# Kernel tuning notes

Hardware: AMD Instinct MI355X
Metric: run time of the kernel (lower is better)

Reference implementation:

```python
import jax, jax.numpy as jnp
import numpy as np

B, G, A = 8, 32768, 64          # molecules, grid points/molecule, atomic orbitals/molecule
N_ORB, DIM, L_FUNC, N_OUT = 400, 128, 3, 1
EPS = 1e-12


def setup_inputs() -> dict:
    key = jax.random.key(0)
    ks = jax.random.split(key, 12)
    # interatomic/grid distances in Bohr-ish range (strictly positive)
    distance_matrices = jax.random.uniform(ks[0], (B, G, A), jnp.float32) * 10.0 + 0.05
    quantum_numbers = jax.random.randint(ks[1], (B, A), 0, 3, jnp.int32)   # q-1 in {0,1,2}
    atomic_orbitals = jax.random.randint(ks[2], (B, A), 0, N_ORB, jnp.int32)
    N_electrons = jax.random.uniform(ks[3], (B,), jnp.float32) * 50.0 + 10.0
    coef_table = jax.random.normal(ks[4], (N_ORB, DIM), jnp.float32) * 0.1
    zeta_table = jnp.ones((N_ORB, 1), jnp.float32)   # nn.init.ones_
    W_pre_w = jax.random.normal(ks[5], (DIM, 1), jnp.float32) * 0.1
    W_pre_b = jax.random.normal(ks[6], (DIM,), jnp.float32) * 0.01
    W_func_w = jax.random.normal(ks[7], (L_FUNC, DIM, DIM), jnp.float32) * (1.0 / np.sqrt(DIM))
    W_func_b = jax.random.normal(ks[8], (L_FUNC, DIM), jnp.float32) * 0.01
    W_prop_w = jax.random.normal(ks[9], (N_OUT, DIM), jnp.float32) * (1.0 / np.sqrt(DIM))
    W_prop_b = jax.random.normal(ks[10], (N_OUT,), jnp.float32) * 0.01
    return dict(distance_matrices=distance_matrices, quantum_numbers=quantum_numbers,
                atomic_orbitals=atomic_orbitals, N_electrons=N_electrons,
                coef_table=coef_table, zeta_table=zeta_table,
                W_pre_w=W_pre_w, W_pre_b=W_pre_b,
                W_func_w=W_func_w, W_func_b=W_func_b,
                W_prop_w=W_prop_w, W_prop_b=W_prop_b)


def reference(distance_matrices, quantum_numbers, atomic_orbitals, N_electrons,
              coef_table, zeta_table, W_pre_w, W_pre_b, W_func_w, W_func_b,
              W_prop_w, W_prop_b):
    d = distance_matrices                                   # [B,G,A]
    q = quantum_numbers.astype(jnp.float32) + 1.0           # principal quantum number {1,2,3}
    z = zeta_table[atomic_orbitals][..., 0]                 # [B,A] orbital exponents
    # GTO basis: d^(q-1) * exp(-(z*d)^2); block-diagonal padding (d=1e6 -> 0) is
    # equivalent to this batched per-molecule form.
    gto = d ** (q[:, None, :] - 1.0) * jnp.exp(-(z[:, None, :] * d) ** 2)
    gto = gto / jnp.maximum(jnp.sqrt(jnp.sum(gto * gto, 1, keepdims=True)), EPS)
    # per-molecule L2-normalized LCAO coefficients (F.normalize over AO axis)
    c = coef_table[atomic_orbitals]                         # [B,A,D]
    c = c / jnp.maximum(jnp.sqrt(jnp.sum(c * c, 1, keepdims=True)), EPS)
    # LCAO: molecular orbitals, then per-molecule normalization over grid points
    mo = jnp.einsum('bga,bad->bgd', gto, c)                 # [B,G,D]
    mo = mo / jnp.maximum(jnp.sqrt(jnp.sum(mo * mo, 1, keepdims=True)), EPS)
    mo = jnp.sqrt(N_electrons / DIM)[:, None, None] * mo
    densities = jnp.sum(mo * mo, -1, keepdims=True)         # [B,G,1]
    # DNN-based energy functional
    v = densities * W_pre_w[:, 0] + W_pre_b                 # [B,G,D]  (Linear(1,dim))
    for l in range(L_FUNC):
        v = jax.nn.relu(jnp.einsum('bgd,ed->bge', v, W_func_w[l]) + W_func_b[l])
    final = jnp.sum(v, 1)                                   # operation == 'sum' over grid
    E_xcH = final @ W_prop_w.T + W_prop_b                   # [B,N_OUT]
    return E_xcH
```

## Files before the change

### kernel.cpp

```cpp
#include <hip/hip_runtime.h>
#include <stdint.h>


#define BB 8
#define GG 32768
#define AA 64
#define DD 128
#define EPSF 1e-12f

#define WS_M    0u
#define WS_ZQ   131072u
#define WS_CN   135168u
#define WS_UW   397312u
#define WS_CCT  398336u
#define WS_W2   529408u
#define WS_W3   562176u
#define WS_DENS 594944u
#define WS_M8   1643520u
#define WS_GTO  2692096u
#define WS_END  36246528u

typedef __attribute__((ext_vector_type(8))) short bf16x8;
typedef __attribute__((ext_vector_type(4))) float f32x4;

__device__ __forceinline__ unsigned short f2bf(float f) {
    union { float f; unsigned int u; } x; x.f = f;
    unsigned int u = x.u + 0x7FFFu + ((x.u >> 16) & 1u);
    return (unsigned short)(u >> 16);
}
__device__ __forceinline__ float bfround(float f) {
    union { float f; unsigned int u; } x; x.f = f;
    unsigned int u = x.u + 0x7FFFu + ((x.u >> 16) & 1u);
    x.u = u & 0xFFFF0000u;
    return x.f;
}
__device__ __forceinline__ float gto_eval(float dv, float zz, float qm) {
    float ttv = zz * dv;
    float ex = __expf(-ttv * ttv);
    float pw = (qm < 0.5f) ? 1.f : ((qm < 1.5f) ? dv : dv * dv);
    return pw * ex;
}

__global__ __launch_bounds__(256)
void k_prep(const int* __restrict__ q, const int* __restrict__ ao,
            const float* __restrict__ coef, const float* __restrict__ zeta,
            const float* __restrict__ wfunc_w, const float* __restrict__ wprop_b,
            float* __restrict__ out, char* __restrict__ ws)
{
    int tid = blockIdx.x * 256 + threadIdx.x;
    if (tid < 32768) {
        int lsel = tid >> 14;
        int idx = tid & 16383;
        unsigned short* dst = (unsigned short*)(ws + (lsel == 0 ? WS_W2 : WS_W3));
        dst[idx] = f2bf(wfunc_w[(lsel + 1) * 16384 + idx]);
    } else if (tid < 33792) {
        int i = tid - 32768;
        int b = i >> 7, dd = i & 127;
        float s = 0.f;
        for (int a = 0; a < AA; ++a) {
            float v = coef[ao[b * AA + a] * DD + dd];
            s += v * v;
        }
        float inv = 1.f / fmaxf(sqrtf(s), EPSF);
        float* cn = (float*)(ws + WS_CN);
        for (int a = 0; a < AA; ++a)
            cn[((size_t)b * AA + a) * DD + dd] = coef[ao[b * AA + a] * DD + dd] * inv;
    } else if (tid < 34304) {
        int i = tid - 33792;
        int b = i >> 6, a = i & 63;
        float* zq = (float*)(ws + WS_ZQ);
        zq[b * 128 + a]      = zeta[ao[b * AA + a]];
        zq[b * 128 + 64 + a] = (float)q[b * AA + a];
    } else if (tid < 34312) {
        out[tid - 34304] = wprop_b[0];
    } else if (tid < 67080) {
        ((float*)(ws + WS_M))[tid - 34312] = 0.f;
    }
}

__global__ __launch_bounds__(1024)
void k_corr2(const float* __restrict__ wpre_w, const float* __restrict__ wpre_b,
             const float* __restrict__ wfunc_w, const float* __restrict__ wfunc_b,
             const float* __restrict__ wprop_w, float* __restrict__ out,
             char* __restrict__ ws)
{
    __shared__ float v1e[128], v1b[128], v2e[128], v2b[128];
    __shared__ float red;
    const int t = threadIdx.x, e = t >> 3, s = t & 7;
    if (t == 0) red = 0.f;
    float* uw = (float*)(ws + WS_UW);

    float su = 0.f, sw = 0.f;
    {
        const float* W1r = wfunc_w + e * 128 + s * 16;
        const float* pw  = wpre_w + s * 16;
        const float* pb  = wpre_b + s * 16;
        #pragma unroll
        for (int k = 0; k < 4; ++k) {
            float4 wv = *(const float4*)(W1r + k * 4);
            float4 a  = *(const float4*)(pw + k * 4);
            float4 bq = *(const float4*)(pb + k * 4);
            su += wv.x * a.x + wv.y * a.y + wv.z * a.z + wv.w * a.w;
            sw += wv.x * bq.x + wv.y * bq.y + wv.z * bq.z + wv.w * bq.w;
        }
    }
    #pragma unroll
    for (int m = 1; m < 8; m <<= 1) { su += __shfl_xor(su, m); sw += __shfl_xor(sw, m); }
    if (s == 0) {
        float w0 = sw + wfunc_b[e];
        uw[e] = su; uw[128 + e] = w0;
        float r = fmaxf(w0, 0.f);
        v1e[e] = r; v1b[e] = bfround(r);
    }
    __syncthreads();

    float ze = 0.f, zb = 0.f;
    {
        const float* W2r = wfunc_w + 16384 + e * 128 + s * 16;
        #pragma unroll
        for (int k = 0; k < 16; ++k) {
            float wv = W2r[k];
            ze += wv * v1e[s * 16 + k];
            zb += bfround(wv) * v1b[s * 16 + k];
        }
    }
    #pragma unroll
    for (int m = 1; m < 8; m <<= 1) { ze += __shfl_xor(ze, m); zb += __shfl_xor(zb, m); }
    if (s == 0) {
        float bias = wfunc_b[128 + e];
        v2e[e] = fmaxf(ze + bias, 0.f);
        v2b[e] = bfround(fmaxf(zb + bias, 0.f));
    }
    __syncthreads();

    float ye = 0.f, yb = 0.f;
    {
        const float* W3r = wfunc_w + 32768 + e * 128 + s * 16;
        #pragma unroll
        for (int k = 0; k < 16; ++k) {
            float wv = W3r[k];
            ye += wv * v2e[s * 16 + k];
            yb += bfround(wv) * v2b[s * 16 + k];
        }
    }
    #pragma unroll
    for (int m = 1; m < 8; m <<= 1) { ye += __shfl_xor(ye, m); yb += __shfl_xor(yb, m); }
    if (s == 0) {
        float bias = wfunc_b[256 + e];
        float diff = (fmaxf(ye + bias, 0.f) - fmaxf(yb + bias, 0.f)) * wprop_w[e];
        atomicAdd(&red, diff);
    }
    __syncthreads();
    if (t == 0) {
        float corr = red * (float)GG;
        #pragma unroll
        for (int b = 0; b < BB; ++b) atomicAdd(&out[b], corr);
    }
}

template<int NREP, bool STORE>
__global__ __launch_bounds__(256, 4)
void k_gto(const float* __restrict__ dmat, char* __restrict__ ws)
{
    __shared__ unsigned short gs[2][8192];
    const int b = blockIdx.y;
    const int chunk = blockIdx.x;
    const int t = threadIdx.x;
    const int g4 = t & 31, a8 = t >> 5;
    const int wv = t >> 6, l = t & 63;
    const int lrow = l & 15, lk = l >> 4;

    const float* zzp = (const float*)(ws + WS_ZQ) + b * 128;
    float4 za = *(const float4*)(zzp + a8 * 8);
    float4 zbv = *(const float4*)(zzp + a8 * 8 + 4);
    float4 qa = *(const float4*)(zzp + 64 + a8 * 8);
    float4 qb = *(const float4*)(zzp + 64 + a8 * 8 + 4);
    float zz8[8] = {za.x, za.y, za.z, za.w, zbv.x, zbv.y, zbv.z, zbv.w};
    float qm8[8] = {qa.x, qa.y, qa.z, qa.w, qb.x, qb.y, qb.z, qb.w};

    const float* dbase = dmat + ((size_t)b * GG + (size_t)chunk * 256) * AA;
    unsigned short* gto = (unsigned short*)(ws + WS_GTO);

    #pragma unroll
    for (int tt = 0; tt < 2; ++tt) {
        float gv[4][8];
        #pragma unroll
        for (int gg = 0; gg < 4; ++gg) {
            const float* rp = dbase + (size_t)(tt * 128 + g4 * 4 + gg) * AA + a8 * 8;
            float4 x0 = *(const float4*)rp;
            float4 x1 = *(const float4*)(rp + 4);
            float dv8[8] = {x0.x, x0.y, x0.z, x0.w, x1.x, x1.y, x1.z, x1.w};
            #pragma unroll
            for (int j = 0; j < 8; ++j) gv[gg][j] = gto_eval(dv8[j], zz8[j], qm8[j]);
        }
        #pragma unroll
        for (int j = 0; j < 8; ++j) {
            int a = a8 * 8 + j;
            unsigned int lo = (unsigned int)f2bf(gv[0][j]) | ((unsigned int)f2bf(gv[1][j]) << 16);
            unsigned int hi = (unsigned int)f2bf(gv[2][j]) | ((unsigned int)f2bf(gv[3][j]) << 16);
            *(uint2*)((char*)gs[tt] + a * 256 + ((g4 * 8) ^ ((a & 15) << 4))) = make_uint2(lo, hi);
        }
        if (STORE) {
            #pragma unroll
            for (int gg = 0; gg < 4; ++gg) {
                unsigned int w0 = (unsigned int)f2bf(gv[gg][0]) | ((unsigned int)f2bf(gv[gg][1]) << 16);
                unsigned int w1 = (unsigned int)f2bf(gv[gg][2]) | ((unsigned int)f2bf(gv[gg][3]) << 16);
                unsigned int w2 = (unsigned int)f2bf(gv[gg][4]) | ((unsigned int)f2bf(gv[gg][5]) << 16);
                unsigned int w3 = (unsigned int)f2bf(gv[gg][6]) | ((unsigned int)f2bf(gv[gg][7]) << 16);
                size_t go = ((size_t)b * GG + (size_t)chunk * 256 + tt * 128 + g4 * 4 + gg) * AA + a8 * 8;
                *(uint4*)(gto + go) = make_uint4(w0, w1, w2, w3);
            }
        }
    }
    __syncthreads();

    f32x4 acc[4];
    #pragma unroll
    for (int rb = 0; rb < 4; ++rb) acc[rb] = (f32x4){0.f, 0.f, 0.f, 0.f};
    #pragma unroll
    for (int tt = 0; tt < 2; ++tt)
        #pragma unroll
        for (int kt = 0; kt < 4; ++kt) {
            int colB = kt * 64 + lk * 16;
            int ra = wv * 16 + lrow;
            bf16x8 af = *(const bf16x8*)((const char*)gs[tt] + ra * 256 + (colB ^ ((ra & 15) << 4)));
            #pragma unroll
            for (int rb = 0; rb < 4; ++rb) {
                int rr = rb * 16 + lrow;
                bf16x8 bv = *(const bf16x8*)((const char*)gs[tt] + rr * 256 + (colB ^ ((rr & 15) << 4)));
                acc[rb] = __builtin_amdgcn_mfma_f32_16x16x32_bf16(af, bv, acc[rb], 0, 0, 0);
            }
        }

    float* Mg = (float*)(ws + (NREP > 1 ? WS_M8 + (unsigned)(chunk & (NREP - 1)) * 131072u
                                        : WS_M)) + b * 4096;
    #pragma unroll
    for (int rb = 0; rb < 4; ++rb)
        #pragma unroll
        for (int r = 0; r < 4; ++r)
            atomicAdd(&Mg[(wv * 16 + lk * 4 + r) * 64 + rb * 16 + lrow], acc[rb][r]);
}

__global__ __launch_bounds__(256)
void k_red(char* __restrict__ ws)
{
    int i = blockIdx.x * 256 + threadIdx.x;
    const float* rp = (const float*)(ws + WS_M8);
    float s = 0.f;
    #pragma unroll
    for (int r = 0; r < 8; ++r) s += rp[r * 32768 + i];
    ((float*)(ws + WS_M))[i] = s;
}

__global__ __launch_bounds__(256)
void k_cct(const float* __restrict__ Ne, char* __restrict__ ws)
{
    __shared__ float M[64][64];
    __shared__ float e_s[128][65];
    __shared__ float inv_na[64];
    __shared__ float alpha[128];
    const int b = blockIdx.x, t = threadIdx.x;
    const float* Mg = (const float*)(ws + WS_M) + b * 4096;
    for (int i = t; i < 4096; i += 256) ((float*)M)[i] = Mg[i];
    __syncthreads();
    if (t < 64) inv_na[t] = 1.f / fmaxf(sqrtf(M[t][t]), EPSF);
    __syncthreads();
    const float* cn = (const float*)(ws + WS_CN) + (size_t)b * AA * DD;
    for (int i = t; i < 8192; i += 256) {
        int a = i >> 7, dd = i & 127;
        e_s[dd][a] = cn[a * DD + dd] * inv_na[a];
    }
    __syncthreads();
    const int d = t >> 1, half = t & 1;
    float y[32];
    #pragma unroll
    for (int j = 0; j < 32; ++j) y[j] = 0.f;
    for (int a = 0; a < 64; ++a) {
        float ea = e_s[d][a];
        const float4* Mr = (const float4*)&M[a][half * 32];
        #pragma unroll 8
        for (int j4 = 0; j4 < 8; ++j4) {
            float4 mv = Mr[j4];
            y[4 * j4 + 0] += ea * mv.x; y[4 * j4 + 1] += ea * mv.y;
            y[4 * j4 + 2] += ea * mv.z; y[4 * j4 + 3] += ea * mv.w;
        }
    }
    float s = 0.f;
    #pragma unroll 8
    for (int j = 0; j < 32; ++j) s += e_s[d][half * 32 + j] * y[j];
    s += __shfl_xor(s, 1);
    if (half == 0) alpha[d] = sqrtf(Ne[b] * (1.f / 128.f)) / fmaxf(sqrtf(s), EPSF);
    __syncthreads();
    unsigned short* cct = (unsigned short*)(ws + WS_CCT) + (size_t)b * 8192;
    for (int i = t; i < 8192; i += 256) {
        int dd = i >> 6, a = i & 63;
        cct[i] = f2bf(e_s[dd][a] * alpha[dd]);
    }
}

template<bool STORE>
__global__ __launch_bounds__(256, 2)
void k_dens(const float* __restrict__ dmat, char* __restrict__ ws)
{
    __shared__ unsigned short ccts[8192];
    const int t = threadIdx.x;
    const int b = blockIdx.x >> 7;
    const int blk = blockIdx.x & 127;
    const int wv = t >> 6, l = t & 63;
    const int lrow = l & 15, lk = l >> 4;

    {
        const uint4* src = (const uint4*)(ws + WS_CCT + (size_t)b * 16384u);
        for (int i = t; i < 1024; i += 256) {
            int off = i * 16;
            int dd = (off >> 7) & 7;
            *(uint4*)((char*)ccts + (off ^ (dd << 4))) = src[i];
        }
    }
    __syncthreads();

    const unsigned short* gto = (const unsigned short*)(ws + WS_GTO);
    float* densp = (float*)(ws + WS_DENS) + (size_t)b * GG;
    const float* zzp = (const float*)(ws + WS_ZQ) + b * 128;

    for (int it = 0; it < 4; ++it) {
        const int g0 = blk * 256 + it * 64 + wv * 16;
        const int g = g0 + lrow;
        f32x4 acc[8];
        #pragma unroll
        for (int j = 0; j < 8; ++j) acc[j] = (f32x4){0.f, 0.f, 0.f, 0.f};
        #pragma unroll
        for (int kt = 0; kt < 2; ++kt) {
            bf16x8 af;
            if (STORE) {
                af = *(const bf16x8*)(gto + ((size_t)b * GG + g) * AA + kt * 32 + lk * 8);
            } else {
                const int a0 = kt * 32 + lk * 8;
                const float* rp = dmat + ((size_t)b * GG + g) * AA + a0;
                float4 x0 = *(const float4*)rp;
                float4 x1 = *(const float4*)(rp + 4);
                float4 z0 = *(const float4*)(zzp + a0);
                float4 z1 = *(const float4*)(zzp + a0 + 4);
                float4 q0 = *(const float4*)(zzp + 64 + a0);
                float4 q1 = *(const float4*)(zzp + 64 + a0 + 4);
                float dv8[8] = {x0.x, x0.y, x0.z, x0.w, x1.x, x1.y, x1.z, x1.w};
                float zz8[8] = {z0.x, z0.y, z0.z, z0.w, z1.x, z1.y, z1.z, z1.w};
                float qm8[8] = {q0.x, q0.y, q0.z, q0.w, q1.x, q1.y, q1.z, q1.w};
                #pragma unroll
                for (int jj = 0; jj < 8; ++jj)
                    af[jj] = (short)f2bf(gto_eval(dv8[jj], zz8[jj], qm8[jj]));
            }
            #pragma unroll
            for (int j = 0; j < 8; ++j) {
                int dr = j * 16 + lrow;
                bf16x8 bv = *(const bf16x8*)((const char*)ccts + dr * 128 +
                                             ((kt * 64 + lk * 16) ^ ((dr & 7) << 4)));
                acc[j] = __builtin_amdgcn_mfma_f32_16x16x32_bf16(af, bv, acc[j], 0, 0, 0);
            }
        }
        float p0 = 0.f, p1 = 0.f, p2 = 0.f, p3 = 0.f;
        #pragma unroll
        for (int j = 0; j < 8; ++j) {
            p0 += acc[j][0] * acc[j][0];
            p1 += acc[j][1] * acc[j][1];
            p2 += acc[j][2] * acc[j][2];
            p3 += acc[j][3] * acc[j][3];
        }
        #pragma unroll
        for (int m = 1; m < 16; m <<= 1) {
            p0 += __shfl_xor(p0, m); p1 += __shfl_xor(p1, m);
            p2 += __shfl_xor(p2, m); p3 += __shfl_xor(p3, m);
        }
        int src = (lrow >> 2) << 4;
        float e0 = __shfl(p0, src), e1 = __shfl(p1, src);
        float e2 = __shfl(p2, src), e3 = __shfl(p3, src);
        int rr = lrow & 3;
        float dv = (rr == 0) ? e0 : (rr == 1) ? e1 : (rr == 2) ? e2 : e3;
        if (lk == 0) densp[g0 + lrow] = dv;
    }
}

#define SMEM_MLP 81920
__global__ __launch_bounds__(256, 2)
void k_mlp(const float* __restrict__ wfunc_b, const float* __restrict__ wprop_w,
           float* __restrict__ out, char* __restrict__ ws)
{
    extern __shared__ char lds[];
    const int t = threadIdx.x;
    const int b = blockIdx.x >> 6;
    const int blk = blockIdx.x & 63;
    const int wv = t >> 6, l = t & 63;
    const int lrow = l & 15, lk = l >> 4;

    {
        const uint4* src = (const uint4*)(ws + WS_W2);
        for (int i = t; i < 4096; i += 256) {
            int off = i * 16;
            int e = (off >> 8) & 7;
            *(uint4*)(lds + (off ^ (e << 4))) = src[i];
        }
    }
    float b2r[8], b3r[8], wpr[8];
    #pragma unroll
    for (int j = 0; j < 8; ++j) {
        b2r[j] = wfunc_b[128 + j * 16 + lrow];
        b3r[j] = wfunc_b[256 + j * 16 + lrow];
        wpr[j] = wprop_w[j * 16 + lrow];
    }
    const float* uwp = (const float*)(ws + WS_UW);
    const float* densp = (const float*)(ws + WS_DENS) + (size_t)b * GG;
    char* vb = lds + 65536 + wv * 4096;
    __syncthreads();

    float esum = 0.f;
    for (int it = 0; it < 4; ++it) {
        const int g0 = blk * 512 + wv * 128 + it * 32;
        float dv0 = densp[g0 + lrow];
        float dv1 = densp[g0 + 16 + lrow];
        f32x4 acc2[2][8];
        #pragma unroll
        for (int i = 0; i < 2; ++i)
            #pragma unroll
            for (int j = 0; j < 8; ++j) acc2[i][j] = (f32x4){0.f, 0.f, 0.f, 0.f};
        #pragma unroll
        for (int kt = 0; kt < 4; ++kt) {
            const int d0 = kt * 32 + lk * 8;
            float4 u0 = *(const float4*)(uwp + d0);
            float4 u1 = *(const float4*)(uwp + d0 + 4);
            float4 w0 = *(const float4*)(uwp + 128 + d0);
            float4 w1 = *(const float4*)(uwp + 128 + d0 + 4);
            float uu[8] = {u0.x, u0.y, u0.z, u0.w, u1.x, u1.y, u1.z, u1.w};
            float ww[8] = {w0.x, w0.y, w0.z, w0.w, w1.x, w1.y, w1.z, w1.w};
            bf16x8 af0, af1;
            #pragma unroll
            for (int jj = 0; jj < 8; ++jj) {
                af0[jj] = (short)f2bf(fmaxf(dv0 * uu[jj] + ww[jj], 0.f));
                af1[jj] = (short)f2bf(fmaxf(dv1 * uu[jj] + ww[jj], 0.f));
            }
            #pragma unroll
            for (int j = 0; j < 8; ++j) {
                int e = j * 16 + lrow;
                bf16x8 bv = *(const bf16x8*)(lds + e * 256 +
                                             ((kt * 64 + lk * 16) ^ ((e & 7) << 4)));
                acc2[0][j] = __builtin_amdgcn_mfma_f32_16x16x32_bf16(af0, bv, acc2[0][j], 0, 0, 0);
                acc2[1][j] = __builtin_amdgcn_mfma_f32_16x16x32_bf16(af1, bv, acc2[1][j], 0, 0, 0);
            }
        }
        #pragma unroll
        for (int h = 0; h < 2; ++h) {
            #pragma unroll
            for (int j = 0; j < 8; ++j) {
                int e = j * 16 + lrow;
                #pragma unroll
                for (int r = 0; r < 4; ++r) {
                    int row = lk * 4 + r;
                    *(unsigned short*)(vb + row * 256 + ((e * 2) ^ ((row & 7) << 4))) =
                        f2bf(fmaxf(acc2[h][j][r] + b2r[j], 0.f));
                }
            }
            f32x4 acc3[8];
            #pragma unroll
            for (int j = 0; j < 8; ++j) acc3[j] = (f32x4){0.f, 0.f, 0.f, 0.f};
            #pragma unroll
            for (int kt = 0; kt < 4; ++kt) {
                bf16x8 af = *(const bf16x8*)(vb + lrow * 256 +
                                             ((kt * 64 + lk * 16) ^ ((lrow & 7) << 4)));
                #pragma unroll
                for (int j = 0; j < 8; ++j) {
                    int e = j * 16 + lrow;
                    bf16x8 bv = *(const bf16x8*)(lds + 32768 + e * 256 +
                                                 ((kt * 64 + lk * 16) ^ ((e & 7) << 4)));
                    acc3[j] = __builtin_amdgcn_mfma_f32_16x16x32_bf16(af, bv, acc3[j], 0, 0, 0);
                }
            }
            #pragma unroll
            for (int j = 0; j < 8; ++j)
                #pragma unroll
                for (int r = 0; r < 4; ++r)
                    esum += fmaxf(acc3[j][r] + b3r[j], 0.f) * wpr[j];
        }
    }
    #pragma unroll
    for (int m = 1; m < 64; m <<= 1) esum += __shfl_xor(esum, m);
    if (l == 0) atomicAdd(&out[b], esum);
}

extern "C" void kernel_launch(void* const* d_in, const int* in_sizes, int n_in,
                              void* d_out, int out_size, void* d_ws, size_t ws_size,
                              hipStream_t stream)
{
    const float* dmat    = (const float*)d_in[0];
    const int*   q       = (const int*)d_in[1];
    const int*   ao      = (const int*)d_in[2];
    const float* Ne      = (const float*)d_in[3];
    const float* coef    = (const float*)d_in[4];
    const float* zeta    = (const float*)d_in[5];
    const float* wpre_w  = (const float*)d_in[6];
    const float* wpre_b  = (const float*)d_in[7];
    const float* wfunc_w = (const float*)d_in[8];
    const float* wfunc_b = (const float*)d_in[9];
    const float* wprop_w = (const float*)d_in[10];
    const float* wprop_b = (const float*)d_in[11];
    float* out = (float*)d_out;
    char*  ws  = (char*)d_ws;

    const bool rep = ws_size >= (size_t)(WS_M8 + 1048576u);
    const bool sg  = ws_size >= (size_t)WS_END;

    k_prep<<<263, 256, 0, stream>>>(q, ao, coef, zeta, wfunc_w, wprop_b, out, ws);
    k_corr2<<<1, 1024, 0, stream>>>(wpre_w, wpre_b, wfunc_w, wfunc_b, wprop_w, out, ws);
    if (rep) {
        hipMemsetAsync(ws + WS_M8, 0, 1048576, stream);
        if (sg) k_gto<8, true><<<dim3(128, BB), 256, 0, stream>>>(dmat, ws);
        else    k_gto<8, false><<<dim3(128, BB), 256, 0, stream>>>(dmat, ws);
        k_red<<<128, 256, 0, stream>>>(ws);
    } else {
        k_gto<1, false><<<dim3(128, BB), 256, 0, stream>>>(dmat, ws);
    }
    k_cct<<<BB, 256, 0, stream>>>(Ne, ws);
    if (sg) k_dens<true><<<1024, 256, 0, stream>>>(dmat, ws);
    else    k_dens<false><<<1024, 256, 0, stream>>>(dmat, ws);
    hipFuncSetAttribute((const void*)k_mlp,
                        hipFuncAttributeMaxDynamicSharedMemorySize, SMEM_MLP);
    k_mlp<<<512, 256, SMEM_MLP, stream>>>(wfunc_b, wprop_w, out, ws);
}
```

Before: 226.9 us.

## Fuse density and MLP kernels, merge prep kernels, replace atomics with partial-sum reduction

Merges the prep and correction kernels into one launch, so one kernel boundary disappears. The GTO Gram matrix is now accumulated into per-chunk partial buffers plus a separate reduction kernel, replacing atomics and the memset, when the workspace is large enough. k_cct is spread over 64 blocks instead of 8. Density computation is fused with the 3-layer MLP, which removes the density round trip through global memory and one launch. In exchange, the MLP weights W2 and W3 are read straight from global memory instead of being staged in LDS, and extra workspace is needed for the partial sums.

```diff
diff --git a/kernel.cpp b/kernel.cpp
--- a/kernel.cpp
+++ b/kernel.cpp
@@ -18,7 +18,9 @@
 #define WS_DENS 594944u
 #define WS_M8   1643520u
 #define WS_GTO  2692096u
-#define WS_END  36246528u
+#define WS_GEND 36246528u
+#define WS_MP   36246528u
+#define WS_MEND 53023744u
 
 typedef __attribute__((ext_vector_type(8))) short bf16x8;
 typedef __attribute__((ext_vector_type(4))) float f32x4;
@@ -41,52 +43,50 @@
     return pw * ex;
 }
 
-__global__ __launch_bounds__(256)
-void k_prep(const int* __restrict__ q, const int* __restrict__ ao,
-            const float* __restrict__ coef, const float* __restrict__ zeta,
-            const float* __restrict__ wfunc_w, const float* __restrict__ wprop_b,
-            float* __restrict__ out, char* __restrict__ ws)
-{
-    int tid = blockIdx.x * 256 + threadIdx.x;
-    if (tid < 32768) {
-        int lsel = tid >> 14;
-        int idx = tid & 16383;
-        unsigned short* dst = (unsigned short*)(ws + (lsel == 0 ? WS_W2 : WS_W3));
-        dst[idx] = f2bf(wfunc_w[(lsel + 1) * 16384 + idx]);
-    } else if (tid < 33792) {
-        int i = tid - 32768;
-        int b = i >> 7, dd = i & 127;
-        float s = 0.f;
-        for (int a = 0; a < AA; ++a) {
-            float v = coef[ao[b * AA + a] * DD + dd];
-            s += v * v;
-        }
-        float inv = 1.f / fmaxf(sqrtf(s), EPSF);
-        float* cn = (float*)(ws + WS_CN);
-        for (int a = 0; a < AA; ++a)
-            cn[((size_t)b * AA + a) * DD + dd] = coef[ao[b * AA + a] * DD + dd] * inv;
-    } else if (tid < 34304) {
-        int i = tid - 33792;
-        int b = i >> 6, a = i & 63;
-        float* zq = (float*)(ws + WS_ZQ);
-        zq[b * 128 + a]      = zeta[ao[b * AA + a]];
-        zq[b * 128 + 64 + a] = (float)q[b * AA + a];
-    } else if (tid < 34312) {
-        out[tid - 34304] = wprop_b[0];
-    } else if (tid < 67080) {
-        ((float*)(ws + WS_M))[tid - 34312] = 0.f;
-    }
-}
-
 __global__ __launch_bounds__(1024)
-void k_corr2(const float* __restrict__ wpre_w, const float* __restrict__ wpre_b,
+void k_prepc(const int* __restrict__ q, const int* __restrict__ ao,
+             const float* __restrict__ coef, const float* __restrict__ zeta,
+             const float* __restrict__ wpre_w, const float* __restrict__ wpre_b,
              const float* __restrict__ wfunc_w, const float* __restrict__ wfunc_b,
-             const float* __restrict__ wprop_w, float* __restrict__ out,
-             char* __restrict__ ws)
-{
+             const float* __restrict__ wprop_w, const float* __restrict__ wprop_b,
+             float* __restrict__ out, char* __restrict__ ws)
+{
+    const int t = threadIdx.x;
+    if (blockIdx.x < 66) {
+        int tid = blockIdx.x * 1024 + t;
+        if (tid < 32768) {
+            int lsel = tid >> 14;
+            int idx = tid & 16383;
+            unsigned short* dst = (unsigned short*)(ws + (lsel == 0 ? WS_W2 : WS_W3));
+            dst[idx] = f2bf(wfunc_w[(lsel + 1) * 16384 + idx]);
+        } else if (tid < 33792) {
+            int i = tid - 32768;
+            int b = i >> 7, dd = i & 127;
+            float s = 0.f;
+            for (int a = 0; a < AA; ++a) {
+                float v = coef[ao[b * AA + a] * DD + dd];
+                s += v * v;
+            }
+            float inv = 1.f / fmaxf(sqrtf(s), EPSF);
+            float* cn = (float*)(ws + WS_CN);
+            for (int a = 0; a < AA; ++a)
+                cn[((size_t)b * AA + a) * DD + dd] = coef[ao[b * AA + a] * DD + dd] * inv;
+        } else if (tid < 34304) {
+            int i = tid - 33792;
+            int b = i >> 6, a = i & 63;
+            float* zq = (float*)(ws + WS_ZQ);
+            zq[b * 128 + a]      = zeta[ao[b * AA + a]];
+            zq[b * 128 + 64 + a] = (float)q[b * AA + a];
+        } else if (tid < 34312) {
+            out[tid - 34304] = wprop_b[0];
+        } else if (tid < 67080) {
+            ((float*)(ws + WS_M))[tid - 34312] = 0.f;
+        }
+        return;
+    }
     __shared__ float v1e[128], v1b[128], v2e[128], v2b[128];
     __shared__ float red;
-    const int t = threadIdx.x, e = t >> 3, s = t & 7;
+    const int e = t >> 3, s = t & 7;
     if (t == 0) red = 0.f;
     float* uw = (float*)(ws + WS_UW);
 
@@ -158,7 +158,7 @@
     }
 }
 
-template<int NREP, bool STORE>
+template<int MODE, bool STORE>
 __global__ __launch_bounds__(256, 4)
 void k_gto(const float* __restrict__ dmat, char* __restrict__ ws)
 {
@@ -232,17 +232,38 @@
             }
         }
 
-    float* Mg = (float*)(ws + (NREP > 1 ? WS_M8 + (unsigned)(chunk & (NREP - 1)) * 131072u
-                                        : WS_M)) + b * 4096;
-    #pragma unroll
-    for (int rb = 0; rb < 4; ++rb)
-        #pragma unroll
-        for (int r = 0; r < 4; ++r)
-            atomicAdd(&Mg[(wv * 16 + lk * 4 + r) * 64 + rb * 16 + lrow], acc[rb][r]);
+    if (MODE == 0) {
+        float* Mp = (float*)(ws + WS_MP) + ((size_t)b * 128 + chunk) * 4096;
+        #pragma unroll
+        for (int rb = 0; rb < 4; ++rb)
+            #pragma unroll
+            for (int r = 0; r < 4; ++r)
+                Mp[(wv * 16 + lk * 4 + r) * 64 + rb * 16 + lrow] = acc[rb][r];
+    } else {
+        float* Mg = (float*)(ws + (MODE == 1 ? WS_M8 + (unsigned)(chunk & 7) * 131072u
+                                             : WS_M)) + b * 4096;
+        #pragma unroll
+        for (int rb = 0; rb < 4; ++rb)
+            #pragma unroll
+            for (int r = 0; r < 4; ++r)
+                atomicAdd(&Mg[(wv * 16 + lk * 4 + r) * 64 + rb * 16 + lrow], acc[rb][r]);
+    }
 }
 
 __global__ __launch_bounds__(256)
-void k_red(char* __restrict__ ws)
+void k_redmp(char* __restrict__ ws)
+{
+    int i = blockIdx.x * 256 + threadIdx.x;
+    int b = i >> 12, idx = i & 4095;
+    const float* p = (const float*)(ws + WS_MP) + (size_t)b * 524288 + idx;
+    float s = 0.f;
+    #pragma unroll 8
+    for (int c = 0; c < 128; ++c) s += p[c * 4096];
+    ((float*)(ws + WS_M))[i] = s;
+}
+
+__global__ __launch_bounds__(256)
+void k_red8(char* __restrict__ ws)
 {
     int i = blockIdx.x * 256 + threadIdx.x;
     const float* rp = (const float*)(ws + WS_M8);
@@ -255,63 +276,67 @@
 __global__ __launch_bounds__(256)
 void k_cct(const float* __restrict__ Ne, char* __restrict__ ws)
 {
-    __shared__ float M[64][64];
-    __shared__ float e_s[128][65];
-    __shared__ float inv_na[64];
-    __shared__ float alpha[128];
-    const int b = blockIdx.x, t = threadIdx.x;
+    __shared__ float Ms[64][68];
+    __shared__ float es[16][64];
+    const int b = blockIdx.x >> 3, dblk = blockIdx.x & 7;
+    const int t = threadIdx.x;
     const float* Mg = (const float*)(ws + WS_M) + b * 4096;
-    for (int i = t; i < 4096; i += 256) ((float*)M)[i] = Mg[i];
-    __syncthreads();
-    if (t < 64) inv_na[t] = 1.f / fmaxf(sqrtf(M[t][t]), EPSF);
-    __syncthreads();
-    const float* cn = (const float*)(ws + WS_CN) + (size_t)b * AA * DD;
-    for (int i = t; i < 8192; i += 256) {
-        int a = i >> 7, dd = i & 127;
-        e_s[dd][a] = cn[a * DD + dd] * inv_na[a];
-    }
-    __syncthreads();
-    const int d = t >> 1, half = t & 1;
-    float y[32];
-    #pragma unroll
-    for (int j = 0; j < 32; ++j) y[j] = 0.f;
+    for (int i = t; i < 4096; i += 256) Ms[i >> 6][i & 63] = Mg[i];
+    __syncthreads();
+    {
+        const float* cn = (const float*)(ws + WS_CN) + (size_t)b * AA * DD;
+        int dl = t & 15, a0 = t >> 4;
+        #pragma unroll
+        for (int p = 0; p < 4; ++p) {
+            int a = p * 16 + a0;
+            float inv = 1.f / fmaxf(sqrtf(Ms[a][a]), EPSF);
+            es[dl][a] = cn[a * DD + dblk * 16 + dl] * inv;
+        }
+    }
+    __syncthreads();
+    const int dl = t >> 4, h = t & 15;
+    float yx = 0.f, yy = 0.f, yz = 0.f, yw = 0.f;
+    #pragma unroll 8
     for (int a = 0; a < 64; ++a) {
-        float ea = e_s[d][a];
-        const float4* Mr = (const float4*)&M[a][half * 32];
-        #pragma unroll 8
-        for (int j4 = 0; j4 < 8; ++j4) {
-            float4 mv = Mr[j4];
-            y[4 * j4 + 0] += ea * mv.x; y[4 * j4 + 1] += ea * mv.y;
-            y[4 * j4 + 2] += ea * mv.z; y[4 * j4 + 3] += ea * mv.w;
-        }
-    }
-    float s = 0.f;
-    #pragma unroll 8
-    for (int j = 0; j < 32; ++j) s += e_s[d][half * 32 + j] * y[j];
-    s += __shfl_xor(s, 1);
-    if (half == 0) alpha[d] = sqrtf(Ne[b] * (1.f / 128.f)) / fmaxf(sqrtf(s), EPSF);
-    __syncthreads();
+        float ea = es[dl][a];
+        float4 m = *(const float4*)&Ms[a][h * 4];
+        yx += ea * m.x; yy += ea * m.y; yz += ea * m.z; yw += ea * m.w;
+    }
+    float4 ev = *(const float4*)&es[dl][h * 4];
+    float s = ev.x * yx + ev.y * yy + ev.z * yz + ev.w * yw;
+    #pragma unroll
+    for (int m = 1; m < 16; m <<= 1) s += __shfl_xor(s, m);
+    float alpha = sqrtf(Ne[b] * (1.f / 128.f)) / fmaxf(sqrtf(s), EPSF);
+    unsigned short q0 = f2bf(es[dl][h * 4 + 0] * alpha);
+    unsigned short q1 = f2bf(es[dl][h * 4 + 1] * alpha);
+    unsigned short q2 = f2bf(es[dl][h * 4 + 2] * alpha);
+    unsigned short q3 = f2bf(es[dl][h * 4 + 3] * alpha);
     unsigned short* cct = (unsigned short*)(ws + WS_CCT) + (size_t)b * 8192;
-    for (int i = t; i < 8192; i += 256) {
-        int dd = i >> 6, a = i & 63;
-        cct[i] = f2bf(e_s[dd][a] * alpha[dd]);
-    }
-}
-
-template<bool STORE>
+    *(uint2*)(cct + (dblk * 16 + dl) * 64 + h * 4) =
+        make_uint2((unsigned)q0 | ((unsigned)q1 << 16), (unsigned)q2 | ((unsigned)q3 << 16));
+}
+
+template<bool SG>
 __global__ __launch_bounds__(256, 2)
-void k_dens(const float* __restrict__ dmat, char* __restrict__ ws)
+void k_fused(const float* __restrict__ dmat, const float* __restrict__ wfunc_b,
+             const float* __restrict__ wprop_w, float* __restrict__ out,
+             char* __restrict__ ws)
 {
     __shared__ unsigned short ccts[8192];
+    __shared__ char v2buf[16384];
+    __shared__ float bsum;
     const int t = threadIdx.x;
-    const int b = blockIdx.x >> 7;
-    const int blk = blockIdx.x & 127;
+    const int b = blockIdx.x >> 8;
+    const int blk = blockIdx.x & 255;
     const int wv = t >> 6, l = t & 63;
     const int lrow = l & 15, lk = l >> 4;
 
+    if (t == 0) bsum = 0.f;
     {
         const uint4* src = (const uint4*)(ws + WS_CCT + (size_t)b * 16384u);
-        for (int i = t; i < 1024; i += 256) {
+        #pragma unroll
+        for (int p = 0; p < 4; ++p) {
+            int i = p * 256 + t;
             int off = i * 16;
             int dd = (off >> 7) & 7;
             *(uint4*)((char*)ccts + (off ^ (dd << 4))) = src[i];
@@ -320,19 +345,23 @@
     __syncthreads();
 
     const unsigned short* gto = (const unsigned short*)(ws + WS_GTO);
-    float* densp = (float*)(ws + WS_DENS) + (size_t)b * GG;
+    const char* W2g = (const char*)ws + WS_W2;
+    const char* W3g = (const char*)ws + WS_W3;
+    const float* uwp = (const float*)(ws + WS_UW);
     const float* zzp = (const float*)(ws + WS_ZQ) + b * 128;
-
-    for (int it = 0; it < 4; ++it) {
-        const int g0 = blk * 256 + it * 64 + wv * 16;
-        const int g = g0 + lrow;
+    const int g0 = blk * 128 + wv * 32;
+
+    float dvh[2];
+    #pragma unroll
+    for (int h = 0; h < 2; ++h) {
+        const int g = g0 + h * 16 + lrow;
         f32x4 acc[8];
         #pragma unroll
         for (int j = 0; j < 8; ++j) acc[j] = (f32x4){0.f, 0.f, 0.f, 0.f};
         #pragma unroll
         for (int kt = 0; kt < 2; ++kt) {
             bf16x8 af;
-            if (STORE) {
+            if (SG) {
                 af = *(const bf16x8*)(gto + ((size_t)b * GG + g) * AA + kt * 32 + lk * 8);
             } else {
                 const int a0 = kt * 32 + lk * 8;
@@ -375,53 +404,17 @@
         float e0 = __shfl(p0, src), e1 = __shfl(p1, src);
         float e2 = __shfl(p2, src), e3 = __shfl(p3, src);
         int rr = lrow & 3;
-        float dv = (rr == 0) ? e0 : (rr == 1) ? e1 : (rr == 2) ? e2 : e3;
-        if (lk == 0) densp[g0 + lrow] = dv;
-    }
-}
-
-#define SMEM_MLP 81920
-__global__ __launch_bounds__(256, 2)
-void k_mlp(const float* __restrict__ wfunc_b, const float* __restrict__ wprop_w,
-           float* __restrict__ out, char* __restrict__ ws)
-{
-    extern __shared__ char lds[];
-    const int t = threadIdx.x;
-    const int b = blockIdx.x >> 6;
-    const int blk = blockIdx.x & 63;
-    const int wv = t >> 6, l = t & 63;
-    const int lrow = l & 15, lk = l >> 4;
-
-    {
-        const uint4* src = (const uint4*)(ws + WS_W2);
-        for (int i = t; i < 4096; i += 256) {
-            int off = i * 16;
-            int e = (off >> 8) & 7;
-            *(uint4*)(lds + (off ^ (e << 4))) = src[i];
-        }
-    }
-    float b2r[8], b3r[8], wpr[8];
-    #pragma unroll
-    for (int j = 0; j < 8; ++j) {
-        b2r[j] = wfunc_b[128 + j * 16 + lrow];
-        b3r[j] = wfunc_b[256 + j * 16 + lrow];
-        wpr[j] = wprop_w[j * 16 + lrow];
-    }
-    const float* uwp = (const float*)(ws + WS_UW);
-    const float* densp = (const float*)(ws + WS_DENS) + (size_t)b * GG;
-    char* vb = lds + 65536 + wv * 4096;
-    __syncthreads();
-
+        dvh[h] = (rr == 0) ? e0 : (rr == 1) ? e1 : (rr == 2) ? e2 : e3;
+    }
+
+    char* vb = v2buf + wv * 4096;
     float esum = 0.f;
-    for (int it = 0; it < 4; ++it) {
-        const int g0 = blk * 512 + wv * 128 + it * 32;
-        float dv0 = densp[g0 + lrow];
-        float dv1 = densp[g0 + 16 + lrow];
-        f32x4 acc2[2][8];
-        #pragma unroll
-        for (int i = 0; i < 2; ++i)
-            #pragma unroll
-            for (int j = 0; j < 8; ++j) acc2[i][j] = (f32x4){0.f, 0.f, 0.f, 0.f};
+    #pragma unroll
+    for (int h = 0; h < 2; ++h) {
+        const float dv = dvh[h];
+        f32x4 acc2[8];
+        #pragma unroll
+        for (int j = 0; j < 8; ++j) acc2[j] = (f32x4){0.f, 0.f, 0.f, 0.f};
         #pragma unroll
         for (int kt = 0; kt < 4; ++kt) {
             const int d0 = kt * 32 + lk * 8;
@@ -431,58 +424,57 @@
             float4 w1 = *(const float4*)(uwp + 128 + d0 + 4);
             float uu[8] = {u0.x, u0.y, u0.z, u0.w, u1.x, u1.y, u1.z, u1.w};
             float ww[8] = {w0.x, w0.y, w0.z, w0.w, w1.x, w1.y, w1.z, w1.w};
-            bf16x8 af0, af1;
-            #pragma unroll
-            for (int jj = 0; jj < 8; ++jj) {
-                af0[jj] = (short)f2bf(fmaxf(dv0 * uu[jj] + ww[jj], 0.f));
-                af1[jj] = (short)f2bf(fmaxf(dv1 * uu[jj] + ww[jj], 0.f));
-            }
+            bf16x8 af;
+            #pragma unroll
+            for (int jj = 0; jj < 8; ++jj)
+                af[jj] = (short)f2bf(fmaxf(dv * uu[jj] + ww[jj], 0.f));
             #pragma unroll
             for (int j = 0; j < 8; ++j) {
                 int e = j * 16 + lrow;
-                bf16x8 bv = *(const bf16x8*)(lds + e * 256 +
-                                             ((kt * 64 + lk * 16) ^ ((e & 7) << 4)));
-                acc2[0][j] = __builtin_amdgcn_mfma_f32_16x16x32_bf16(af0, bv, acc2[0][j], 0, 0, 0);
-                acc2[1][j] = __builtin_amdgcn_mfma_f32_16x16x32_bf16(af1, bv, acc2[1][j], 0, 0, 0);
-            }
-        }
-        #pragma unroll
-        for (int h = 0; h < 2; ++h) {
+                bf16x8 bv = *(const bf16x8*)(W2g + e * 256 + kt * 64 + lk * 16);
+                acc2[j] = __builtin_amdgcn_mfma_f32_16x16x32_bf16(af, bv, acc2[j], 0, 0, 0);
+            }
+        }
+        #pragma unroll
+        for (int j = 0; j < 8; ++j) {
+            int e = j * 16 + lrow;
+            float bias = wfunc_b[128 + e];
+            #pragma unroll
+            for (int r = 0; r < 4; ++r) {
+                int row = lk * 4 + r;
+                *(unsigned short*)(vb + row * 256 + ((e * 2) ^ ((row & 7) << 4))) =
+                    f2bf(fmaxf(acc2[j][r] + bias, 0.f));
+            }
+        }
+        f32x4 acc3[8];
+        #pragma unroll
+        for (int j = 0; j < 8; ++j) acc3[j] = (f32x4){0.f, 0.f, 0.f, 0.f};
+        #pragma unroll
+        for (int kt = 0; kt < 4; ++kt) {
+            bf16x8 af = *(const bf16x8*)(vb + lrow * 256 +
+                                         ((kt * 64 + lk * 16) ^ ((lrow & 7) << 4)));
             #pragma unroll
             for (int j = 0; j < 8; ++j) {
                 int e = j * 16 + lrow;
-                #pragma unroll
-                for (int r = 0; r < 4; ++r) {
-                    int row = lk * 4 + r;
-                    *(unsigned short*)(vb + row * 256 + ((e * 2) ^ ((row & 7) << 4))) =
-                        f2bf(fmaxf(acc2[h][j][r] + b2r[j], 0.f));
-                }
-            }
-            f32x4 acc3[8];
-            #pragma unroll
-            for (int j = 0; j < 8; ++j) acc3[j] = (f32x4){0.f, 0.f, 0.f, 0.f};
-            #pragma unroll
-            for (int kt = 0; kt < 4; ++kt) {
-                bf16x8 af = *(const bf16x8*)(vb + lrow * 256 +
-                                             ((kt * 64 + lk * 16) ^ ((lrow & 7) << 4)));
-                #pragma unroll
-                for (int j = 0; j < 8; ++j) {
-                    int e = j * 16 + lrow;
-                    bf16x8 bv = *(const bf16x8*)(lds + 32768 + e * 256 +
-                                                 ((kt * 64 + lk * 16) ^ ((e & 7) << 4)));
-                    acc3[j] = __builtin_amdgcn_mfma_f32_16x16x32_bf16(af, bv, acc3[j], 0, 0, 0);
-                }
-            }
-            #pragma unroll
-            for (int j = 0; j < 8; ++j)
-                #pragma unroll
-                for (int r = 0; r < 4; ++r)
-                    esum += fmaxf(acc3[j][r] + b3r[j], 0.f) * wpr[j];
+                bf16x8 bv = *(const bf16x8*)(W3g + e * 256 + kt * 64 + lk * 16);
+                acc3[j] = __builtin_amdgcn_mfma_f32_16x16x32_bf16(af, bv, acc3[j], 0, 0, 0);
+            }
+        }
+        #pragma unroll
+        for (int j = 0; j < 8; ++j) {
+            int e = j * 16 + lrow;
+            float bias = wfunc_b[256 + e], wpv = wprop_w[e];
+            #pragma unroll
+            for (int r = 0; r < 4; ++r)
+                esum += fmaxf(acc3[j][r] + bias, 0.f) * wpv;
         }
     }
     #pragma unroll
     for (int m = 1; m < 64; m <<= 1) esum += __shfl_xor(esum, m);
-    if (l == 0) atomicAdd(&out[b], esum);
+    __syncthreads();
+    if (l == 0) atomicAdd(&bsum, esum);
+    __syncthreads();
+    if (t == 0) atomicAdd(&out[b], bsum);
 }
 
 extern "C" void kernel_launch(void* const* d_in, const int* in_sizes, int n_in,
@@ -504,23 +496,22 @@
     float* out = (float*)d_out;
     char*  ws  = (char*)d_ws;
 
-    const bool rep = ws_size >= (size_t)(WS_M8 + 1048576u);
-    const bool sg  = ws_size >= (size_t)WS_END;
-
-    k_prep<<<263, 256, 0, stream>>>(q, ao, coef, zeta, wfunc_w, wprop_b, out, ws);
-    k_corr2<<<1, 1024, 0, stream>>>(wpre_w, wpre_b, wfunc_w, wfunc_b, wprop_w, out, ws);
-    if (rep) {
+    const bool sg = ws_size >= (size_t)WS_GEND;
+    const bool mp = ws_size >= (size_t)WS_MEND;
+
+    k_prepc<<<67, 1024, 0, stream>>>(q, ao, coef, zeta, wpre_w, wpre_b,
+                                     wfunc_w, wfunc_b, wprop_w, wprop_b, out, ws);
+    if (mp) {
+        k_gto<0, true><<<dim3(128, BB), 256, 0, stream>>>(dmat, ws);
+        k_redmp<<<128, 256, 0, stream>>>(ws);
+    } else if (sg) {
         hipMemsetAsync(ws + WS_M8, 0, 1048576, stream);
-        if (sg) k_gto<8, true><<<dim3(128, BB), 256, 0, stream>>>(dmat, ws);
-        else    k_gto<8, false><<<dim3(128, BB), 256, 0, stream>>>(dmat, ws);
-        k_red<<<128, 256, 0, stream>>>(ws);
+        k_gto<1, true><<<dim3(128, BB), 256, 0, stream>>>(dmat, ws);
+        k_red8<<<128, 256, 0, stream>>>(ws);
     } else {
-        k_gto<1, false><<<dim3(128, BB), 256, 0, stream>>>(dmat, ws);
-    }
-    k_cct<<<BB, 256, 0, stream>>>(Ne, ws);
-    if (sg) k_dens<true><<<1024, 256, 0, stream>>>(dmat, ws);
-    else    k_dens<false><<<1024, 256, 0, stream>>>(dmat, ws);
-    hipFuncSetAttribute((const void*)k_mlp,
-                        hipFuncAttributeMaxDynamicSharedMemorySize, SMEM_MLP);
-    k_mlp<<<512, 256, SMEM_MLP, stream>>>(wfunc_b, wprop_w, out, ws);
-}
+        k_gto<2, false><<<dim3(128, BB), 256, 0, stream>>>(dmat, ws);
+    }
+    k_cct<<<64, 256, 0, stream>>>(Ne, ws);
+    if (sg) k_fused<true><<<2048, 256, 0, stream>>>(dmat, wfunc_b, wprop_w, out, ws);
+    else    k_fused<false><<<2048, 256, 0, stream>>>(dmat, wfunc_b, wprop_w, out, ws);
+}
```

Result: slower. 330.4 us (+45.6%).
